# Kernel tuning notes

Hardware: AMD Instinct MI355X
Metric: run time of the kernel (lower is better)

## Reference

```python
import jax, jax.numpy as jnp
import numpy as np

LN_EPS = 1e-5

def _layer_norm(x, g, b):
    m = jnp.mean(x, axis=-1, keepdims=True)
    v = jnp.mean(jnp.square(x - m), axis=-1, keepdims=True)
    return (x - m) * jax.lax.rsqrt(v + LN_EPS) * g + b

def setup_inputs() -> dict:
    key = jax.random.key(0)
    ks = jax.random.split(key, 12)
    n_views, n_pts, nnz = 2000, 100000, 1000000
    F_sp = F_view = F_g = 256
    F_in = F_out = 128
    return {
        "scenepoint_features": jax.random.normal(ks[0], (n_pts, F_sp), jnp.float32),
        "view_features": jax.random.normal(ks[1], (n_views, F_view), jnp.float32),
        "global_features": jax.random.normal(ks[2], (1, F_g), jnp.float32),
        "proj_values": jax.random.normal(ks[3], (nnz, F_in), jnp.float32),
        "view_idx": jax.random.randint(ks[4], (nnz,), 0, n_views, jnp.int32),
        "pt_idx": jax.random.randint(ks[5], (nnz,), 0, n_pts, jnp.int32),
        "ln_sp_g": jnp.ones((F_sp,), jnp.float32),
        "ln_sp_b": jnp.zeros((F_sp,), jnp.float32),
        "ln_view_g": jnp.ones((F_view,), jnp.float32),
        "ln_view_b": jnp.zeros((F_view,), jnp.float32),
        "ln_g_g": jnp.ones((F_g,), jnp.float32),
        "ln_g_b": jnp.zeros((F_g,), jnp.float32),
        "W_proj": jax.random.normal(ks[6], (F_out, F_in), jnp.float32) * 0.02,
        "b_proj": jnp.zeros((F_out,), jnp.float32),
        "W_sp": jax.random.normal(ks[7], (F_out, F_sp), jnp.float32) * 0.02,
        "W_view": jax.random.normal(ks[8], (F_out, F_view), jnp.float32) * 0.02,
        "W_g": jax.random.normal(ks[9], (F_out, F_g), jnp.float32) * 0.02,
    }

def reference(scenepoint_features, view_features, global_features, proj_values,
              view_idx, pt_idx,
              ln_sp_g, ln_sp_b, ln_view_g, ln_view_b, ln_g_g, ln_g_b,
              W_proj, b_proj, W_sp, W_view, W_g):
    # normalize + relu global/node features
    sp = jax.nn.relu(_layer_norm(scenepoint_features, ln_sp_g, ln_sp_b))
    vw = jax.nn.relu(_layer_norm(view_features, ln_view_g, ln_view_b))
    gl = jax.nn.relu(_layer_norm(global_features, ln_g_g, ln_g_b))
    # linear projections (small dense GEMMs on node tables, big one on nnz values)
    proj = proj_values @ W_proj.T + b_proj              # [nnz, F_out]
    sp_p = sp @ W_sp.T                                  # [n_pts, F_out]
    vw_p = vw @ W_view.T                                # [n_views, F_out]
    gl_p = gl @ W_g.T                                   # [1, F_out]
    # sparse gather + combine
    new_features = (proj + sp_p[pt_idx] + vw_p[view_idx] + gl_p) * 0.25
    return new_features
```

## Files before the change

kernel.cpp:

```cpp
#include <hip/hip_runtime.h>
#include <hip/hip_bf16.h>

#define LN_EPS 1e-5f

typedef float  f32x4  __attribute__((ext_vector_type(4)));
typedef short  bf16x8 __attribute__((ext_vector_type(8)));

static __device__ __forceinline__ short f2bf(float x) {
    unsigned u = __float_as_uint(x);
    unsigned r = (u + 0x7fffu + ((u >> 16) & 1u)) >> 16;
    return (short)r;
}

#define SWZ(r, b) ((b) ^ (((r) & 7) << 4))

__global__ void k_prep(const float* __restrict__ Wp, const float* __restrict__ Ws,
                       const float* __restrict__ Wv, short* __restrict__ wbuf) {
    int i = blockIdx.x * 256 + threadIdx.x;
    if (i < 16384)      wbuf[i] = f2bf(Wp[i]);
    else if (i < 49152) wbuf[i] = f2bf(Ws[i - 16384]);
    else if (i < 81920) wbuf[i] = f2bf(Wv[i - 49152]);
}

__global__ void k_bias(const float* __restrict__ gf, const float* __restrict__ gg,
                       const float* __restrict__ gb, const float* __restrict__ Wg,
                       const float* __restrict__ bp, float* __restrict__ bias) {
    __shared__ float sm[256];
    __shared__ float red[8];
    int t = threadIdx.x;
    float x = gf[t];
    float s = x;
    #pragma unroll
    for (int o = 32; o > 0; o >>= 1) s += __shfl_xor(s, o, 64);
    if ((t & 63) == 0) red[t >> 6] = s;
    __syncthreads();
    float m = (red[0] + red[1] + red[2] + red[3]) * (1.0f / 256.0f);
    float d = x - m;
    float q = d * d;
    #pragma unroll
    for (int o = 32; o > 0; o >>= 1) q += __shfl_xor(q, o, 64);
    if ((t & 63) == 0) red[4 + (t >> 6)] = q;
    __syncthreads();
    float v = (red[4] + red[5] + red[6] + red[7]) * (1.0f / 256.0f);
    float n = fmaxf(d * rsqrtf(v + LN_EPS) * gg[t] + gb[t], 0.0f);
    sm[t] = n;
    __syncthreads();
    if (t < 128) {
        float acc = bp[t];
        const float* wrow = Wg + t * 256;
        #pragma unroll 8
        for (int k = 0; k < 256; ++k) acc = fmaf(sm[k], wrow[k], acc);
        bias[t] = acc;
    }
}

__global__ __launch_bounds__(256) void k_ln_gemm(
    const float* __restrict__ A, const float* __restrict__ g, const float* __restrict__ b,
    const short* __restrict__ Wb, float* __restrict__ out, int M)
{
    __shared__ char smem[65536];
    char* As = smem;
    char* Wc = smem + 32768;

    const int t  = threadIdx.x;
    const int l  = t & 63;
    const int w  = t >> 6;
    const int rb = blockIdx.x * 64;

    {
        int lr  = w * 16 + (l >> 2);
        int row = min(rb + lr, M - 1);
        const float* src = A + (size_t)row * 256 + (l & 3) * 64;
        float s = 0.f, s2 = 0.f;
        #pragma unroll
        for (int j = 0; j < 16; ++j) {
            f32x4 v = ((const f32x4*)src)[j];
            s  += v.x + v.y + v.z + v.w;
            s2 += v.x * v.x + v.y * v.y + v.z * v.z + v.w * v.w;
        }
        s  += __shfl_xor(s, 1, 64);  s  += __shfl_xor(s, 2, 64);
        s2 += __shfl_xor(s2, 1, 64); s2 += __shfl_xor(s2, 2, 64);
        float mean = s * (1.0f / 256.0f);
        float var  = s2 * (1.0f / 256.0f) - mean * mean;
        float inv  = rsqrtf(var + LN_EPS);
        const float* gp = g + (l & 3) * 64;
        const float* bp = b + (l & 3) * 64;
        char* arow = As + lr * 512;
        #pragma unroll
        for (int j = 0; j < 8; ++j) {
            f32x4 v0 = ((const f32x4*)src)[2 * j];
            f32x4 v1 = ((const f32x4*)src)[2 * j + 1];
            f32x4 g0 = ((const f32x4*)gp)[2 * j];
            f32x4 g1 = ((const f32x4*)gp)[2 * j + 1];
            f32x4 b0 = ((const f32x4*)bp)[2 * j];
            f32x4 b1 = ((const f32x4*)bp)[2 * j + 1];
            bf16x8 pack;
            pack[0] = f2bf(fmaxf((v0.x - mean) * inv * g0.x + b0.x, 0.f));
            pack[1] = f2bf(fmaxf((v0.y - mean) * inv * g0.y + b0.y, 0.f));
            pack[2] = f2bf(fmaxf((v0.z - mean) * inv * g0.z + b0.z, 0.f));
            pack[3] = f2bf(fmaxf((v0.w - mean) * inv * g0.w + b0.w, 0.f));
            pack[4] = f2bf(fmaxf((v1.x - mean) * inv * g1.x + b1.x, 0.f));
            pack[5] = f2bf(fmaxf((v1.y - mean) * inv * g1.y + b1.y, 0.f));
            pack[6] = f2bf(fmaxf((v1.z - mean) * inv * g1.z + b1.z, 0.f));
            pack[7] = f2bf(fmaxf((v1.w - mean) * inv * g1.w + b1.w, 0.f));
            int boff = (l & 3) * 128 + j * 16;
            *(bf16x8*)(arow + SWZ(lr, boff)) = pack;
        }
    }
    __syncthreads();

    f32x4 acc[8];
    #pragma unroll
    for (int i = 0; i < 8; ++i) acc[i] = (f32x4){0.f, 0.f, 0.f, 0.f};

    const int arow_l = w * 16 + (l & 15);
    const char* abase = As + arow_l * 512;

    for (int h = 0; h < 2; ++h) {
        const char* wsrc = (const char*)(Wb + h * 64 * 256);
        #pragma unroll
        for (int i = 0; i < 8; ++i) {
            int c = t + i * 256;
            int lrow = c >> 5;
            int boff = (c & 31) * 16;
            bf16x8 val = *(const bf16x8*)(wsrc + lrow * 512 + boff);
            *(bf16x8*)(Wc + lrow * 512 + SWZ(lrow, boff)) = val;
        }
        __syncthreads();

        #pragma unroll
        for (int kc = 0; kc < 8; ++kc) {
            int kb = kc * 64 + (l >> 4) * 16;
            bf16x8 af = *(const bf16x8*)(abase + SWZ(arow_l, kb));
            #pragma unroll
            for (int nt = 0; nt < 4; ++nt) {
                int lrow = nt * 16 + (l & 15);
                bf16x8 wf = *(const bf16x8*)(Wc + lrow * 512 + SWZ(lrow, kb));
                acc[h * 4 + nt] = __builtin_amdgcn_mfma_f32_16x16x32_bf16(wf, af, acc[h * 4 + nt], 0, 0, 0);
            }
        }
        __syncthreads();
    }

    const int orow = rb + w * 16 + (l & 15);
    if (orow < M) {
        float* orp = out + (size_t)orow * 128;
        #pragma unroll
        for (int h = 0; h < 2; ++h)
            #pragma unroll
            for (int nt = 0; nt < 4; ++nt) {
                int c0 = h * 64 + nt * 16 + (l >> 4) * 4;
                *(f32x4*)(orp + c0) = acc[h * 4 + nt];
            }
    }
}

__global__ __launch_bounds__(512) void k_main(
    const float* __restrict__ pv, const int* __restrict__ vidx, const int* __restrict__ pidx,
    const short* __restrict__ Wp, const float* __restrict__ bias,
    const float* __restrict__ spp, const float* __restrict__ vwp,
    float* __restrict__ out, int M, int ntiles)
{
    __shared__ char Wc[32768];
    __shared__ float bias_s[128];
    const int t  = threadIdx.x;
    const int l  = t & 63;
    const int w  = t >> 6;

    #pragma unroll
    for (int i = 0; i < 4; ++i) {
        int c = t + i * 512;
        int row = c >> 4;
        int boff = (c & 15) * 16;
        bf16x8 val = *(const bf16x8*)((const char*)Wp + row * 256 + boff);
        *(bf16x8*)(Wc + row * 256 + SWZ(row, boff)) = val;
    }
    if (t < 128) bias_s[t] = bias[t];
    __syncthreads();

    for (int tile = blockIdx.x; tile < ntiles; tile += gridDim.x) {
        const int rb    = tile * 128;
        const int row_l = rb + w * 16 + (l & 15);
        const int orow  = min(row_l, M - 1);
        const int pt = pidx[orow];
        const int vw = vidx[orow];

        f32x4 acc[8];
        #pragma unroll
        for (int i = 0; i < 8; ++i) acc[i] = (f32x4){0.f, 0.f, 0.f, 0.f};

        const float* arow_g = pv + (size_t)orow * 128;

        #pragma unroll
        for (int kc = 0; kc < 4; ++kc) {
            int k0 = kc * 32 + (l >> 4) * 8;
            f32x4 a0 = __builtin_nontemporal_load((const f32x4*)(arow_g + k0));
            f32x4 a1 = __builtin_nontemporal_load((const f32x4*)(arow_g + k0 + 4));
            bf16x8 af;
            af[0] = f2bf(a0.x); af[1] = f2bf(a0.y); af[2] = f2bf(a0.z); af[3] = f2bf(a0.w);
            af[4] = f2bf(a1.x); af[5] = f2bf(a1.y); af[6] = f2bf(a1.z); af[7] = f2bf(a1.w);
            #pragma unroll
            for (int nt = 0; nt < 8; ++nt) {
                int lrow = nt * 16 + (l & 15);
                bf16x8 wf = *(const bf16x8*)(Wc + lrow * 256 + SWZ(lrow, k0 * 2));
                acc[nt] = __builtin_amdgcn_mfma_f32_16x16x32_bf16(wf, af, acc[nt], 0, 0, 0);
            }
        }

        if (row_l < M) {
            const float* spr = spp + (size_t)pt * 128;
            const float* vwr = vwp + (size_t)vw * 128;
            float* orp = out + (size_t)orow * 128;
            #pragma unroll
            for (int nt = 0; nt < 8; ++nt) {
                int c0 = nt * 16 + (l >> 4) * 4;
                f32x4 sp4 = *(const f32x4*)(spr + c0);
                f32x4 vw4 = *(const f32x4*)(vwr + c0);
                f32x4 b4  = *(const f32x4*)(bias_s + c0);
                f32x4 r   = acc[nt];
                r = (r + sp4 + vw4 + b4) * 0.25f;
                __builtin_nontemporal_store(r, (f32x4*)(orp + c0));
            }
        }
    }
}

extern "C" void kernel_launch(void* const* d_in, const int* in_sizes, int n_in,
                              void* d_out, int out_size, void* d_ws, size_t ws_size,
                              hipStream_t stream) {
    const float* sp_f    = (const float*)d_in[0];
    const float* vw_f    = (const float*)d_in[1];
    const float* gl_f    = (const float*)d_in[2];
    const float* pv      = (const float*)d_in[3];
    const int*   vidx    = (const int*)d_in[4];
    const int*   pidx    = (const int*)d_in[5];
    const float* ln_sp_g = (const float*)d_in[6];
    const float* ln_sp_b = (const float*)d_in[7];
    const float* ln_vw_g = (const float*)d_in[8];
    const float* ln_vw_b = (const float*)d_in[9];
    const float* ln_g_g  = (const float*)d_in[10];
    const float* ln_g_b  = (const float*)d_in[11];
    const float* W_proj  = (const float*)d_in[12];
    const float* b_proj  = (const float*)d_in[13];
    const float* W_sp    = (const float*)d_in[14];
    const float* W_view  = (const float*)d_in[15];
    const float* W_g     = (const float*)d_in[16];

    const int n_pts   = in_sizes[0] / 256;
    const int n_views = in_sizes[1] / 256;
    const int nnz     = in_sizes[3] / 128;

    short* wbuf = (short*)d_ws;
    float* bias = (float*)((char*)d_ws + 163840);
    float* spp  = (float*)((char*)d_ws + 164352);
    float* vwp  = (float*)((char*)d_ws + 164352 + (size_t)n_pts * 128 * 4);

    k_prep<<<320, 256, 0, stream>>>(W_proj, W_sp, W_view, wbuf);
    k_bias<<<1, 256, 0, stream>>>(gl_f, ln_g_g, ln_g_b, W_g, b_proj, bias);
    k_ln_gemm<<<(n_pts + 63) / 64, 256, 0, stream>>>(sp_f, ln_sp_g, ln_sp_b, wbuf + 16384, spp, n_pts);
    k_ln_gemm<<<(n_views + 63) / 64, 256, 0, stream>>>(vw_f, ln_vw_g, ln_vw_b, wbuf + 49152, vwp, n_views);

    const int ntiles = (nnz + 127) / 128;
    int grid = ntiles < 1024 ? ntiles : 1024;
    k_main<<<grid, 512, 0, stream>>>(pv, vidx, pidx, wbuf, bias, spp, vwp, (float*)d_out, nnz, ntiles);
}
```

Baseline: 424.0 us.

## Prefetch next tile gather indices and interleave MFMA with epilogue per column tile

Result: slower. 756.8 us (+78.5%).

```diff
diff --git a/kernel.cpp b/kernel.cpp
--- a/kernel.cpp
+++ b/kernel.cpp
@@ -155,7 +155,7 @@
     }
 }
 
-__global__ __launch_bounds__(512) void k_main(
+__global__ __launch_bounds__(512, 6) void k_main(
     const float* __restrict__ pv, const int* __restrict__ vidx, const int* __restrict__ pidx,
     const short* __restrict__ Wp, const float* __restrict__ bias,
     const float* __restrict__ spp, const float* __restrict__ vwp,
@@ -178,50 +178,67 @@
     if (t < 128) bias_s[t] = bias[t];
     __syncthreads();
 
-    for (int tile = blockIdx.x; tile < ntiles; tile += gridDim.x) {
-        const int rb    = tile * 128;
-        const int row_l = rb + w * 16 + (l & 15);
+    const int lane_r = w * 16 + (l & 15);
+    const int q      = (l >> 4);
+
+    int tile = blockIdx.x;
+    int pt_c = 0, vw_c = 0;
+    if (tile < ntiles) {
+        int orow0 = min(tile * 128 + lane_r, M - 1);
+        pt_c = pidx[orow0];
+        vw_c = vidx[orow0];
+    }
+
+    for (; tile < ntiles; tile += gridDim.x) {
+        const int row_l = tile * 128 + lane_r;
         const int orow  = min(row_l, M - 1);
-        const int pt = pidx[orow];
-        const int vw = vidx[orow];
-
-        f32x4 acc[8];
-        #pragma unroll
-        for (int i = 0; i < 8; ++i) acc[i] = (f32x4){0.f, 0.f, 0.f, 0.f};
+
+        int pt_n = 0, vw_n = 0;
+        {
+            int nxt = tile + gridDim.x;
+            if (nxt < ntiles) {
+                int orown = min(nxt * 128 + lane_r, M - 1);
+                pt_n = pidx[orown];
+                vw_n = vidx[orown];
+            }
+        }
 
         const float* arow_g = pv + (size_t)orow * 128;
-
+        bf16x8 af[4];
         #pragma unroll
         for (int kc = 0; kc < 4; ++kc) {
-            int k0 = kc * 32 + (l >> 4) * 8;
+            int k0 = kc * 32 + q * 8;
             f32x4 a0 = __builtin_nontemporal_load((const f32x4*)(arow_g + k0));
             f32x4 a1 = __builtin_nontemporal_load((const f32x4*)(arow_g + k0 + 4));
-            bf16x8 af;
-            af[0] = f2bf(a0.x); af[1] = f2bf(a0.y); af[2] = f2bf(a0.z); af[3] = f2bf(a0.w);
-            af[4] = f2bf(a1.x); af[5] = f2bf(a1.y); af[6] = f2bf(a1.z); af[7] = f2bf(a1.w);
+            af[kc][0] = f2bf(a0.x); af[kc][1] = f2bf(a0.y); af[kc][2] = f2bf(a0.z); af[kc][3] = f2bf(a0.w);
+            af[kc][4] = f2bf(a1.x); af[kc][5] = f2bf(a1.y); af[kc][6] = f2bf(a1.z); af[kc][7] = f2bf(a1.w);
+        }
+
+        const float* spr = spp + (size_t)pt_c * 128;
+        const float* vwr = vwp + (size_t)vw_c * 128;
+        float* orp = out + (size_t)orow * 128;
+        const bool ok = (row_l < M);
+
+        #pragma unroll
+        for (int nt = 0; nt < 8; ++nt) {
+            f32x4 acc = (f32x4){0.f, 0.f, 0.f, 0.f};
             #pragma unroll
-            for (int nt = 0; nt < 8; ++nt) {
+            for (int kc = 0; kc < 4; ++kc) {
+                int kb = kc * 64 + q * 16;
                 int lrow = nt * 16 + (l & 15);
-                bf16x8 wf = *(const bf16x8*)(Wc + lrow * 256 + SWZ(lrow, k0 * 2));
-                acc[nt] = __builtin_amdgcn_mfma_f32_16x16x32_bf16(wf, af, acc[nt], 0, 0, 0);
-            }
-        }
-
-        if (row_l < M) {
-            const float* spr = spp + (size_t)pt * 128;
-            const float* vwr = vwp + (size_t)vw * 128;
-            float* orp = out + (size_t)orow * 128;
-            #pragma unroll
-            for (int nt = 0; nt < 8; ++nt) {
-                int c0 = nt * 16 + (l >> 4) * 4;
-                f32x4 sp4 = *(const f32x4*)(spr + c0);
-                f32x4 vw4 = *(const f32x4*)(vwr + c0);
-                f32x4 b4  = *(const f32x4*)(bias_s + c0);
-                f32x4 r   = acc[nt];
-                r = (r + sp4 + vw4 + b4) * 0.25f;
-                __builtin_nontemporal_store(r, (f32x4*)(orp + c0));
-            }
-        }
+                bf16x8 wf = *(const bf16x8*)(Wc + lrow * 256 + SWZ(lrow, kb));
+                acc = __builtin_amdgcn_mfma_f32_16x16x32_bf16(wf, af[kc], acc, 0, 0, 0);
+            }
+            int c0 = nt * 16 + q * 4;
+            f32x4 sp4 = *(const f32x4*)(spr + c0);
+            f32x4 vw4 = *(const f32x4*)(vwr + c0);
+            f32x4 b4  = *(const f32x4*)(bias_s + c0);
+            f32x4 r = (acc + sp4 + vw4 + b4) * 0.25f;
+            if (ok) __builtin_nontemporal_store(r, (f32x4*)(orp + c0));
+        }
+
+        pt_c = pt_n;
+        vw_c = vw_n;
     }
 }
 
```
